# Optimization experiments

Hardware: AMD Instinct MI355X
Metric: run time of the kernel (lower is better)

Reference implementation:

```python
import jax, jax.numpy as jnp
import numpy as np

N, E, FIN, H, OUT, L = 80000, 1280000, 128, 64, 10, 3
NEG_SLOPE = 0.2


def setup_inputs() -> dict:
    key = jax.random.key(0)
    ks = jax.random.split(key, 2 + 6 * L + 2)
    inp = {
        "x": jax.random.normal(ks[0], (N, FIN), dtype=jnp.float32),
        "edge_index": jax.random.randint(ks[1], (2, E), 0, N, dtype=jnp.int32),
        "batch": jnp.zeros((N,), dtype=jnp.int32),
    }
    k = 2
    for l in range(L):
        fin = FIN if l == 0 else H
        s = 1.0 / np.sqrt(fin)
        inp[f"Wl{l}"] = jax.random.normal(ks[k + 0], (H, fin), dtype=jnp.float32) * s
        inp[f"bl{l}"] = jnp.zeros((H,), dtype=jnp.float32)
        inp[f"Wr{l}"] = jax.random.normal(ks[k + 1], (H, fin), dtype=jnp.float32) * s
        inp[f"br{l}"] = jnp.zeros((H,), dtype=jnp.float32)
        inp[f"att{l}"] = jax.random.normal(ks[k + 2], (H,), dtype=jnp.float32) * (1.0 / np.sqrt(H))
        inp[f"b{l}"] = jnp.zeros((H,), dtype=jnp.float32)
        k += 3
    inp["Wro"] = jax.random.normal(ks[k], (OUT, H), dtype=jnp.float32) * (1.0 / np.sqrt(H))
    inp["bro"] = jnp.zeros((OUT,), dtype=jnp.float32)
    return inp


def gatv2_layer(h, src, dst, Wl, bl, Wr, br, att, b):
    # PyG GATv2Conv (heads=1, share_weights=False):
    #   xl = lin_l(h) (source side), xr = lin_r(h) (target side)
    xl = h @ Wl.T + bl          # [N, H]
    xr = h @ Wr.T + br          # [N, H]
    e = jax.nn.leaky_relu(xl[src] + xr[dst], NEG_SLOPE) @ att  # [E_tot]
    # softmax over incoming edges of each destination node
    m = jax.ops.segment_max(e, dst, num_segments=N)
    ex = jnp.exp(e - m[dst])
    denom = jax.ops.segment_sum(ex, dst, num_segments=N)
    alpha = ex / denom[dst]
    out = jax.ops.segment_sum(alpha[:, None] * xl[src], dst, num_segments=N)
    return out + b


def reference(x, edge_index, batch,
              Wl0, bl0, Wr0, br0, att0, b0,
              Wl1, bl1, Wr1, br1, att1, b1,
              Wl2, bl2, Wr2, br2, att2, b2,
              Wro, bro):
    # add self-loops once (same augmented edge set used each layer)
    loop = jnp.arange(N, dtype=edge_index.dtype)
    src = jnp.concatenate([edge_index[0], loop])
    dst = jnp.concatenate([edge_index[1], loop])
    layers = [
        (Wl0, bl0, Wr0, br0, att0, b0),
        (Wl1, bl1, Wr1, br1, att1, b1),
        (Wl2, bl2, Wr2, br2, att2, b2),
    ]
    h = x
    for (Wl, bl, Wr, br, att, b) in layers:
        h = jax.nn.relu(gatv2_layer(h, src, dst, Wl, bl, Wr, br, att, b))
    # graph_level_task=False: node-level readout
    return h @ Wro.T + bro  # [N, OUT]
```

## Files before the change

kernel.cpp:

```cpp
#include <hip/hip_runtime.h>
#include <hip/hip_bf16.h>
#include <hip/hip_fp16.h>


#define NN 80000
#define EE 1280000
#define FIN 128
#define HH 64
#define OUTD 10
#define NBUK 79
#define PCH 2048
#define NCH 625

typedef __hip_bfloat16 bf16;
typedef _Float16 f16x8 __attribute__((ext_vector_type(8)));
typedef float f32x4 __attribute__((ext_vector_type(4)));

__device__ __forceinline__ float ldw(const void* p, int i, int f) {
    return f ? __bfloat162float(((const bf16*)p)[i]) : ((const float*)p)[i];
}

__global__ void detect_kernel(const unsigned* __restrict__ w, int* __restrict__ flag) {
    int lane = threadIdx.x;
    int big = 0;
    for (int i = lane; i < 2048; i += 64) {
        unsigned u = w[i];
        float a = __uint_as_float(u << 16);
        float b = __uint_as_float(u & 0xffff0000u);
        if (!(fabsf(a) <= 1024.f)) big = 1;
        if (!(fabsf(b) <= 1024.f)) big = 1;
    }
    big = (__ballot(big) != 0ull) ? 1 : 0;
    if (lane == 0) flag[0] = big ? 0 : 1;
}

__global__ void preconvert(
    const void* Wl0, const void* Wr0, const void* Wl1, const void* Wr1,
    const void* Wl2, const void* Wr2,
    const void* bl0, const void* br0, const void* bl1, const void* br1,
    const void* bl2, const void* br2,
    const void* att0, const void* att1, const void* att2,
    const void* b0, const void* b1, const void* b2,
    const void* Wro, const void* bro,
    __half* Wh0, __half* Wh1, __half* Wh2, float* small,
    const int* __restrict__ flagp)
{
    const int f = flagp[0];
    int t = blockIdx.x * 256 + threadIdx.x;
    if (t < 16384) {
        int j = t & 127, k = t >> 7;
        float v = (j < 64) ? ldw(Wl0, j * 128 + k, f) : ldw(Wr0, (j - 64) * 128 + k, f);
        Wh0[j * 128 + k] = __float2half(v);
    } else if (t < 24576) {
        int u = t - 16384; int j = u & 127, k = u >> 7;
        float v = (j < 64) ? ldw(Wl1, j * 64 + k, f) : ldw(Wr1, (j - 64) * 64 + k, f);
        Wh1[j * 64 + k] = __float2half(v);
    } else if (t < 32768) {
        int u = t - 24576; int j = u & 127, k = u >> 7;
        float v = (j < 64) ? ldw(Wl2, j * 64 + k, f) : ldw(Wr2, (j - 64) * 64 + k, f);
        Wh2[j * 64 + k] = __float2half(v);
    } else if (t < 34304) {
        int s = t - 32768;
        const void* BL[3] = { bl0, bl1, bl2 };
        const void* BR[3] = { br0, br1, br2 };
        const void* AT[3] = { att0, att1, att2 };
        const void* BB[3] = { b0, b1, b2 };
        float v = 0.f;
        if (s < 384) {
            int l = s / 128, r = s % 128;
            v = (r < 64) ? ldw(BL[l], r, f) : ldw(BR[l], r - 64, f);
        } else if (s < 576) {
            int q = s - 384; v = ldw(AT[q / 64], q % 64, f);
        } else if (s < 768) {
            int q = s - 576; v = ldw(BB[q / 64], q % 64, f);
        } else if (s < 1408) {
            v = ldw(Wro, s - 768, f);
        } else if (s < 1418) {
            v = ldw(bro, s - 1408, f);
        } else return;
        small[s] = v;
    }
}

__global__ __launch_bounds__(256) void chunkhist_kernel(const int* __restrict__ dst,
                                                        int* __restrict__ chunkcnt)
{
    __shared__ int h[NBUK];
    const int tid = threadIdx.x, c = blockIdx.x;
    for (int i = tid; i < NBUK; i += 256) h[i] = 0;
    __syncthreads();
    const int e0 = c * PCH + tid * 8;
    int4 a = *(const int4*)(dst + e0);
    int4 b = *(const int4*)(dst + e0 + 4);
    atomicAdd(&h[a.x >> 10], 1); atomicAdd(&h[a.y >> 10], 1);
    atomicAdd(&h[a.z >> 10], 1); atomicAdd(&h[a.w >> 10], 1);
    atomicAdd(&h[b.x >> 10], 1); atomicAdd(&h[b.y >> 10], 1);
    atomicAdd(&h[b.z >> 10], 1); atomicAdd(&h[b.w >> 10], 1);
    __syncthreads();
    for (int i = tid; i < NBUK; i += 256) chunkcnt[i * NCH + c] = h[i];
}

__global__ __launch_bounds__(1024) void cscan_kernel(int* __restrict__ chunkcnt,
                                                     int* __restrict__ bucket_cnt)
{
    __shared__ int s[1024];
    const int b = blockIdx.x, t = threadIdx.x;
    int v = (t < NCH) ? chunkcnt[b * NCH + t] : 0;
    s[t] = v;
    __syncthreads();
    #pragma unroll
    for (int off = 1; off < 1024; off <<= 1) {
        int u = (t >= off) ? s[t - off] : 0;
        __syncthreads();
        s[t] += u;
        __syncthreads();
    }
    if (t < NCH) chunkcnt[b * NCH + t] = s[t] - v;
    if (t == NCH - 1) bucket_cnt[b] = s[t];
}

__global__ void bscan_kernel(const int* __restrict__ bucket_cnt,
                             int* __restrict__ bucket_base)
{
    __shared__ int sc[128];
    const int t = threadIdx.x;
    sc[t] = (t < NBUK) ? bucket_cnt[t] : 0;
    __syncthreads();
    #pragma unroll
    for (int off = 1; off < 128; off <<= 1) {
        int v = (t >= off) ? sc[t - off] : 0;
        __syncthreads();
        sc[t] += v;
        __syncthreads();
    }
    if (t < NBUK) bucket_base[t] = (t == 0) ? 0 : sc[t - 1];
    if (t == 0) bucket_base[NBUK] = sc[NBUK - 1];
}

__global__ __launch_bounds__(256) void part_kernel(const int* __restrict__ src,
                                                   const int* __restrict__ dst,
                                                   const int* __restrict__ chunkcnt,
                                                   const int* __restrict__ bucket_base,
                                                   int2* __restrict__ part)
{
    __shared__ int hcnt[NBUK];
    __shared__ int sc[128];
    __shared__ int hbase[NBUK + 1];
    __shared__ int hpos[NBUK];
    __shared__ int hgb[NBUK];
    __shared__ int2 stage[PCH];
    const int tid = threadIdx.x, c = blockIdx.x;

    for (int i = tid; i < NBUK; i += 256) hcnt[i] = 0;
    __syncthreads();

    const int e0 = c * PCH + tid * 8;
    int4 sa = *(const int4*)(src + e0);
    int4 sb = *(const int4*)(src + e0 + 4);
    int4 da = *(const int4*)(dst + e0);
    int4 db = *(const int4*)(dst + e0 + 4);
    int dv[8] = { da.x, da.y, da.z, da.w, db.x, db.y, db.z, db.w };
    int sv[8] = { sa.x, sa.y, sa.z, sa.w, sb.x, sb.y, sb.z, sb.w };
    #pragma unroll
    for (int u = 0; u < 8; u++) atomicAdd(&hcnt[dv[u] >> 10], 1);
    __syncthreads();

    if (tid < 128) sc[tid] = (tid < NBUK) ? hcnt[tid] : 0;
    __syncthreads();
    #pragma unroll
    for (int off = 1; off < 128; off <<= 1) {
        int v = (tid < 128 && tid >= off) ? sc[tid - off] : 0;
        __syncthreads();
        if (tid < 128) sc[tid] += v;
        __syncthreads();
    }
    if (tid < NBUK) {
        int b = (tid == 0) ? 0 : sc[tid - 1];
        hbase[tid] = b;
        hpos[tid] = b;
        hgb[tid] = bucket_base[tid] + chunkcnt[tid * NCH + c];
    }
    if (tid == 0) hbase[NBUK] = PCH;
    __syncthreads();

    #pragma unroll
    for (int u = 0; u < 8; u++) {
        int p = atomicAdd(&hpos[dv[u] >> 10], 1);
        stage[p] = make_int2(sv[u], dv[u]);
    }
    __syncthreads();

    for (int s = tid; s < PCH; s += 256) {
        int lo = 0, hi = NBUK;
        #pragma unroll
        for (int it = 0; it < 7; it++) {
            int mid = (lo + hi) >> 1;
            if (hbase[mid] <= s) lo = mid; else hi = mid;
        }
        part[hgb[lo] + (s - hbase[lo])] = stage[s];
    }
}

__global__ __launch_bounds__(256) void hist_part_kernel(const int2* __restrict__ part,
                                                        const int* __restrict__ bucket_base,
                                                        int* __restrict__ cnt)
{
    __shared__ int lcnt[1024];
    const int b = blockIdx.x, tid = threadIdx.x;
    const int dbase = b << 10;
    for (int i = tid; i < 1024; i += 256) lcnt[i] = 0;
    __syncthreads();
    const int eb = bucket_base[b], ee = bucket_base[b + 1];
    for (int e = eb + tid; e < ee; e += 256)
        atomicAdd(&lcnt[part[e].y - dbase], 1);
    __syncthreads();
    const int nd = min(1024, NN - dbase);
    for (int i = tid; i < nd; i += 256) cnt[dbase + i] = lcnt[i];
}

__global__ void scan1(const int* __restrict__ cnt, int* __restrict__ rowptr,
                      int* __restrict__ bsums) {
    __shared__ int sh[256];
    int i = blockIdx.x * 256 + threadIdx.x;
    int tid = threadIdx.x;
    int c = (i < NN) ? cnt[i] : 0;
    sh[tid] = c;
    __syncthreads();
    #pragma unroll
    for (int off = 1; off < 256; off <<= 1) {
        int t = (tid >= off) ? sh[tid - off] : 0;
        __syncthreads();
        sh[tid] += t;
        __syncthreads();
    }
    if (i < NN) rowptr[i + 1] = sh[tid];
    if (tid == 255) bsums[blockIdx.x] = sh[255];
}

__global__ void scan2(int* __restrict__ bsums, int nb) {
    __shared__ int sh[512];
    int t = threadIdx.x;
    sh[t] = (t < nb) ? bsums[t] : 0;
    __syncthreads();
    #pragma unroll
    for (int off = 1; off < 512; off <<= 1) {
        int v = (t >= off) ? sh[t - off] : 0;
        __syncthreads();
        sh[t] += v;
        __syncthreads();
    }
    if (t < nb) bsums[t] = sh[t];
}

__global__ void scan3(int* __restrict__ rowptr, const int* __restrict__ bsums) {
    int i = blockIdx.x * 256 + threadIdx.x;
    if (i == 0) rowptr[0] = 0;
    int add = (blockIdx.x == 0) ? 0 : bsums[blockIdx.x - 1];
    if (i < NN) rowptr[i + 1] += add;
}

__global__ __launch_bounds__(256) void scatter2_kernel(const int2* __restrict__ part,
                                                       const int* __restrict__ bucket_base,
                                                       const int* __restrict__ rowptr,
                                                       int* __restrict__ col)
{
    __shared__ int lfill[1024];
    const int b = blockIdx.x, tid = threadIdx.x;
    const int dbase = b << 10;
    const int nd = min(1024, NN - dbase);
    for (int i = tid; i < nd; i += 256) lfill[i] = rowptr[dbase + i];
    __syncthreads();
    const int eb = bucket_base[b], ee = bucket_base[b + 1];
    for (int e = eb + tid; e < ee; e += 256) {
        int2 sd = part[e];
        int pos = atomicAdd(&lfill[sd.y - dbase], 1);
        col[pos] = sd.x;
    }
}

#define ELX_S 72
#define EXR_S 68
template<int F, bool L0>
__global__ __launch_bounds__(256) void lin_mfma(const void* __restrict__ hin_,
                                                const __half* __restrict__ Wh,
                                                const float* __restrict__ biasLR,
                                                const float* __restrict__ attf,
                                                __half* __restrict__ xlh,
                                                float* __restrict__ xr,
                                                float* __restrict__ slp,
                                                float* __restrict__ srp,
                                                const int* __restrict__ flagp)
{
    __shared__ __align__(16) char lds[64 * ELX_S * 2 + 64 * EXR_S * 4];
    _Float16* xs  = (_Float16*)lds;
    _Float16* eXL = (_Float16*)lds;
    float*    eXR = (float*)(lds + 64 * ELX_S * 2);

    const int tid = threadIdx.x;
    const int nb = blockIdx.x * 64;
    constexpr int OPR = F / 8;

    if (L0 && flagp[0]) {
        const uint4* hp = (const uint4*)hin_;
        for (int c = tid; c < 64 * OPR; c += 256) {
            int row = c / OPR, oct = c % OPR;
            uint4 u = hp[((size_t)(nb + row) * F + oct * 8) >> 3];
            unsigned ww[4] = { u.x, u.y, u.z, u.w };
            _Float16 v[8];
            #pragma unroll
            for (int p = 0; p < 4; p++) {
                v[2 * p]     = (_Float16)__uint_as_float(ww[p] << 16);
                v[2 * p + 1] = (_Float16)__uint_as_float(ww[p] & 0xffff0000u);
            }
            int so = oct ^ (row & 7);
            *(f16x8*)&xs[row * F + so * 8] = *(f16x8*)v;
        }
    } else {
        const float4* hp = (const float4*)hin_;
        for (int c = tid; c < 64 * OPR; c += 256) {
            int row = c / OPR, oct = c % OPR;
            size_t base = ((size_t)(nb + row) * F + oct * 8) >> 2;
            float4 a = hp[base], b = hp[base + 1];
            _Float16 v[8] = { (_Float16)a.x, (_Float16)a.y, (_Float16)a.z, (_Float16)a.w,
                              (_Float16)b.x, (_Float16)b.y, (_Float16)b.z, (_Float16)b.w };
            int so = oct ^ (row & 7);
            *(f16x8*)&xs[row * F + so * 8] = *(f16x8*)v;
        }
    }
    __syncthreads();

    const int w = tid >> 6;
    const int lane = tid & 63;
    const int n = lane & 15;
    const int quad = lane >> 4;
    constexpr int NS = F / 32;

    f16x8 afr[NS];
    #pragma unroll
    for (int s = 0; s < NS; s++) {
        int o = (s * 4 + quad) ^ (n & 7);
        afr[s] = *(const f16x8*)&xs[(w * 16 + n) * F + o * 8];
    }
    __syncthreads();

    const _Float16* Whf = (const _Float16*)Wh;
    #pragma unroll
    for (int ct = 0; ct < 8; ct++) {
        float bv = biasLR[ct * 16 + n];
        f32x4 acc = { bv, bv, bv, bv };
        #pragma unroll
        for (int s = 0; s < NS; s++) {
            f16x8 bfr = *(const f16x8*)&Whf[(size_t)(ct * 16 + n) * F + s * 32 + quad * 8];
            acc = __builtin_amdgcn_mfma_f32_16x16x32_f16(afr[s], bfr, acc, 0, 0, 0);
        }
        int rbase = w * 16 + quad * 4;
        if (ct < 4) {
            #pragma unroll
            for (int rg = 0; rg < 4; rg++)
                eXL[(rbase + rg) * ELX_S + ct * 16 + n] = (_Float16)acc[rg];
        } else {
            #pragma unroll
            for (int rg = 0; rg < 4; rg++)
                eXR[(rbase + rg) * EXR_S + (ct - 4) * 16 + n] = acc[rg];
        }
    }
    __syncthreads();

    for (int c = tid; c < 512; c += 256) {
        int row = c >> 3, oct = c & 7;
        *(uint4*)&xlh[(size_t)(nb + row) * 64 + oct * 8] =
            *(const uint4*)&eXL[row * ELX_S + oct * 8];
    }
    for (int c = tid; c < 1024; c += 256) {
        int row = c >> 4, q4 = c & 15;
        *(float4*)&xr[(size_t)(nb + row) * 64 + q4 * 4] =
            *(const float4*)&eXR[row * EXR_S + q4 * 4];
    }

    if (tid < 64) {
        float accl = 0.f, accr = 0.f;
        #pragma unroll
        for (int o = 0; o < 8; o++) {
            f16x8 vl = *(const f16x8*)&eXL[tid * ELX_S + o * 8];
            float4 a0 = *(const float4*)(attf + o * 8);
            float4 a1 = *(const float4*)(attf + o * 8 + 4);
            float4 v0 = *(const float4*)&eXR[tid * EXR_S + o * 8];
            float4 v1 = *(const float4*)&eXR[tid * EXR_S + o * 8 + 4];
            accl = fmaf(a0.x, (float)vl[0], accl);
            accl = fmaf(a0.y, (float)vl[1], accl);
            accl = fmaf(a0.z, (float)vl[2], accl);
            accl = fmaf(a0.w, (float)vl[3], accl);
            accl = fmaf(a1.x, (float)vl[4], accl);
            accl = fmaf(a1.y, (float)vl[5], accl);
            accl = fmaf(a1.z, (float)vl[6], accl);
            accl = fmaf(a1.w, (float)vl[7], accl);
            accr = fmaf(a0.x, v0.x, accr);
            accr = fmaf(a0.y, v0.y, accr);
            accr = fmaf(a0.z, v0.z, accr);
            accr = fmaf(a0.w, v0.w, accr);
            accr = fmaf(a1.x, v1.x, accr);
            accr = fmaf(a1.y, v1.y, accr);
            accr = fmaf(a1.z, v1.z, accr);
            accr = fmaf(a1.w, v1.w, accr);
        }
        slp[nb + tid] = accl;
        srp[nb + tid] = accr;
    }
}

#define DECODE8(U, D) { \
    float2 _f0 = __half22float2(*(__half2*)&U.x); \
    float2 _f1 = __half22float2(*(__half2*)&U.y); \
    float2 _f2 = __half22float2(*(__half2*)&U.z); \
    float2 _f3 = __half22float2(*(__half2*)&U.w); \
    D[0]=_f0.x; D[1]=_f0.y; D[2]=_f1.x; D[3]=_f1.y; \
    D[4]=_f2.x; D[5]=_f2.y; D[6]=_f3.x; D[7]=_f3.y; }

__global__ __launch_bounds__(256) void agg6_kernel(const __half* __restrict__ xlh,
                                                   const float* __restrict__ xr,
                                                   const float* __restrict__ slp,
                                                   const float* __restrict__ srp,
                                                   const float* __restrict__ attf,
                                                   const float* __restrict__ bf,
                                                   const int* __restrict__ rowptr,
                                                   const int* __restrict__ col,
                                                   float* __restrict__ hout)
{
    const int lane = threadIdx.x & 63;
    const int g = lane >> 3;
    const int r = lane & 7;
    const int wid = blockIdx.x * 4 + (threadIdx.x >> 6);
    const int i = wid * 8 + g;

    float xri[8], att[8];
    {
        float4 xa = *(const float4*)(xr + (size_t)i * 64 + r * 8);
        float4 xb = *(const float4*)(xr + (size_t)i * 64 + r * 8 + 4);
        xri[0]=xa.x; xri[1]=xa.y; xri[2]=xa.z; xri[3]=xa.w;
        xri[4]=xb.x; xri[5]=xb.y; xri[6]=xb.z; xri[7]=xb.w;
        float4 aa = *(const float4*)(attf + r * 8);
        float4 ab = *(const float4*)(attf + r * 8 + 4);
        att[0]=aa.x; att[1]=aa.y; att[2]=aa.z; att[3]=aa.w;
        att[4]=ab.x; att[5]=ab.y; att[6]=ab.z; att[7]=ab.w;
    }
    const float sri06 = 0.6f * srp[i];

    uint4 srow = *(const uint4*)(xlh + (size_t)i * 64 + r * 8);
    float s[8]; DECODE8(srow, s);
    float ps = 0.f;
    #pragma unroll
    for (int k = 0; k < 8; k++)
        ps = fmaf(att[k], fabsf(s[k] + xri[k]), ps);
    ps += __shfl_xor(ps, 1, 64);
    ps += __shfl_xor(ps, 2, 64);
    ps += __shfl_xor(ps, 4, 64);
    float es = fmaf(0.4f, ps, fmaf(0.6f, slp[i], sri06));
    float wself = __expf(fminf(es, 60.f));

    float acc[8];
    #pragma unroll
    for (int k = 0; k < 8; k++) acc[k] = wself * s[k];
    float denom = wself;

    const int e0 = rowptr[i], e1 = rowptr[i + 1];

    int e = e0;
    for (; e + 2 <= e1; e += 2) {
        int sa = col[e];
        int sb = col[e + 1];
        float sla = slp[sa], slb = slp[sb];
        uint4 ua = *(const uint4*)(xlh + (size_t)sa * 64 + r * 8);
        uint4 ub = *(const uint4*)(xlh + (size_t)sb * 64 + r * 8);
        float A[8], B[8];
        DECODE8(ua, A);
        DECODE8(ub, B);

        float pa = 0.f, pb = 0.f;
        #pragma unroll
        for (int k = 0; k < 8; k++) {
            pa = fmaf(att[k], fabsf(A[k] + xri[k]), pa);
            pb = fmaf(att[k], fabsf(B[k] + xri[k]), pb);
        }
        pa += __shfl_xor(pa, 1, 64);  pb += __shfl_xor(pb, 1, 64);
        pa += __shfl_xor(pa, 2, 64);  pb += __shfl_xor(pb, 2, 64);
        pa += __shfl_xor(pa, 4, 64);  pb += __shfl_xor(pb, 4, 64);

        float ea = fmaf(0.4f, pa, fmaf(0.6f, sla, sri06));
        float eb = fmaf(0.4f, pb, fmaf(0.6f, slb, sri06));
        float wa = __expf(fminf(ea, 60.f));
        float wb = __expf(fminf(eb, 60.f));

        #pragma unroll
        for (int k = 0; k < 8; k++) {
            acc[k] = fmaf(wa, A[k], acc[k]);
            acc[k] = fmaf(wb, B[k], acc[k]);
        }
        denom += wa + wb;
    }
    if (e < e1) {
        int sa = col[e];
        float sla = slp[sa];
        uint4 ua = *(const uint4*)(xlh + (size_t)sa * 64 + r * 8);
        float A[8];
        DECODE8(ua, A);

        float pa = 0.f;
        #pragma unroll
        for (int k = 0; k < 8; k++)
            pa = fmaf(att[k], fabsf(A[k] + xri[k]), pa);
        pa += __shfl_xor(pa, 1, 64);
        pa += __shfl_xor(pa, 2, 64);
        pa += __shfl_xor(pa, 4, 64);

        float ea = fmaf(0.4f, pa, fmaf(0.6f, sla, sri06));
        float wa = __expf(fminf(ea, 60.f));

        #pragma unroll
        for (int k = 0; k < 8; k++)
            acc[k] = fmaf(wa, A[k], acc[k]);
        denom += wa;
    }

    float inv = 1.f / denom;
    float4 bfa = *(const float4*)(bf + r * 8);
    float4 bfb = *(const float4*)(bf + r * 8 + 4);
    float o0 = fmaxf(fmaf(acc[0], inv, bfa.x), 0.f);
    float o1 = fmaxf(fmaf(acc[1], inv, bfa.y), 0.f);
    float o2 = fmaxf(fmaf(acc[2], inv, bfa.z), 0.f);
    float o3 = fmaxf(fmaf(acc[3], inv, bfa.w), 0.f);
    float o4 = fmaxf(fmaf(acc[4], inv, bfb.x), 0.f);
    float o5 = fmaxf(fmaf(acc[5], inv, bfb.y), 0.f);
    float o6 = fmaxf(fmaf(acc[6], inv, bfb.z), 0.f);
    float o7 = fmaxf(fmaf(acc[7], inv, bfb.w), 0.f);
    float* op = hout + (size_t)i * 64 + r * 8;
    *(float4*)(op)     = make_float4(o0, o1, o2, o3);
    *(float4*)(op + 4) = make_float4(o4, o5, o6, o7);
}

__global__ __launch_bounds__(256) void readout2_kernel(const float* __restrict__ h,
                                                       const float* __restrict__ WROf,
                                                       const float* __restrict__ brof,
                                                       void* __restrict__ out,
                                                       const int* __restrict__ flagp)
{
    __shared__ float wsh[640];
    __shared__ float bsh[OUTD];
    const int tid = threadIdx.x;
    for (int idx = tid; idx < 640; idx += 256) {
        int k = idx / 10, o = idx % 10;
        wsh[idx] = WROf[o * 64 + k];
    }
    if (tid < OUTD) bsh[tid] = brof[tid];
    __syncthreads();

    const int i = blockIdx.x * 256 + tid;
    if (i >= NN) return;
    const int f = flagp[0];

    float res[OUTD];
    #pragma unroll
    for (int o = 0; o < OUTD; o++) res[o] = bsh[o];

    const float4* h4 = (const float4*)(h + (size_t)i * 64);
    #pragma unroll 4
    for (int c = 0; c < 16; c++) {
        float4 hv = h4[c];
        const float* wp = &wsh[c * 40];
        #pragma unroll
        for (int o = 0; o < OUTD; o++) {
            float t = fmaf(hv.x, wp[o], fmaf(hv.y, wp[10 + o],
                      fmaf(hv.z, wp[20 + o], hv.w * wp[30 + o])));
            res[o] += t;
        }
    }

    if (f) {
        bf16* op = (bf16*)out + (size_t)i * OUTD;
        #pragma unroll
        for (int o = 0; o < OUTD; o++) op[o] = __float2bfloat16(res[o]);
    } else {
        float* op = (float*)out + (size_t)i * OUTD;
        #pragma unroll
        for (int o = 0; o < OUTD; o++) op[o] = res[o];
    }
}

extern "C" void kernel_launch(void* const* d_in, const int* in_sizes, int n_in,
                              void* d_out, int out_size, void* d_ws, size_t ws_size,
                              hipStream_t stream) {
    const void* x   = d_in[0];
    const int* ei   = (const int*)d_in[1];
    const void* Wl0 = d_in[3];  const void* bl0 = d_in[4];
    const void* Wr0 = d_in[5];  const void* br0 = d_in[6];
    const void* at0 = d_in[7];  const void* b0  = d_in[8];
    const void* Wl1 = d_in[9];  const void* bl1 = d_in[10];
    const void* Wr1 = d_in[11]; const void* br1 = d_in[12];
    const void* at1 = d_in[13]; const void* b1  = d_in[14];
    const void* Wl2 = d_in[15]; const void* bl2 = d_in[16];
    const void* Wr2 = d_in[17]; const void* br2 = d_in[18];
    const void* at2 = d_in[19]; const void* b2  = d_in[20];
    const void* Wro = d_in[21]; const void* bro = d_in[22];

    const int* srcArr = ei;
    const int* dstArr = ei + EE;

    float* wf = (float*)d_ws;
    __half* Wh0  = (__half*)wf;
    __half* Wh1  = (__half*)(wf + 16384);
    __half* Wh2  = (__half*)(wf + 24576);
    float* small = wf + 32768;
    int*   flag  = (int*)(wf + 34304);
    int*   rowptr = (int*)(wf + 34368);
    int*   bsums  = (int*)(wf + 114496);
    int*   fillc  = (int*)(wf + 115008);
    int*   bucket_cnt  = (int*)(wf + 195008);
    int*   bucket_base = (int*)(wf + 195136);
    int*   chunkcnt    = (int*)(wf + 195264);
    int2*  part   = (int2*)(wf + 244736);
    int*   col    = (int*)(wf + 2804736);
    float* slp    = wf + 4084736;
    float* srp    = wf + 4164736;
    __half* xlh   = (__half*)(wf + 5364736);
    float* xr = wf + 7924736;
    float* hA = xr + (size_t)NN * 64;

    float* biasLR0 = small;        float* biasLR1 = small + 128; float* biasLR2 = small + 256;
    float* attf0 = small + 384;    float* attf1 = small + 448;   float* attf2 = small + 512;
    float* bf0   = small + 576;    float* bf1   = small + 640;   float* bf2   = small + 704;
    float* WROf  = small + 768;    float* brof  = small + 1408;

    detect_kernel<<<dim3(1), dim3(64), 0, stream>>>((const unsigned*)Wl0, flag);

    preconvert<<<dim3(134), dim3(256), 0, stream>>>(
        Wl0, Wr0, Wl1, Wr1, Wl2, Wr2, bl0, br0, bl1, br1, bl2, br2,
        at0, at1, at2, b0, b1, b2, Wro, bro, Wh0, Wh1, Wh2, small, flag);

    chunkhist_kernel<<<dim3(NCH), dim3(256), 0, stream>>>(dstArr, chunkcnt);
    cscan_kernel<<<dim3(NBUK), dim3(1024), 0, stream>>>(chunkcnt, bucket_cnt);
    bscan_kernel<<<dim3(1), dim3(128), 0, stream>>>(bucket_cnt, bucket_base);
    part_kernel<<<dim3(NCH), dim3(256), 0, stream>>>(srcArr, dstArr, chunkcnt, bucket_base, part);
    hist_part_kernel<<<dim3(NBUK), dim3(256), 0, stream>>>(part, bucket_base, fillc);
    scan1<<<dim3(313), dim3(256), 0, stream>>>(fillc, rowptr, bsums);
    scan2<<<dim3(1), dim3(512), 0, stream>>>(bsums, 313);
    scan3<<<dim3(313), dim3(256), 0, stream>>>(rowptr, bsums);
    scatter2_kernel<<<dim3(NBUK), dim3(256), 0, stream>>>(part, bucket_base, rowptr, col);

    lin_mfma<128, true><<<dim3(NN / 64), dim3(256), 0, stream>>>(x, Wh0, biasLR0, attf0, xlh, xr, slp, srp, flag);
    agg6_kernel<<<dim3(NN / 32), dim3(256), 0, stream>>>(xlh, xr, slp, srp, attf0, bf0, rowptr, col, hA);
    lin_mfma<64, false><<<dim3(NN / 64), dim3(256), 0, stream>>>(hA, Wh1, biasLR1, attf1, xlh, xr, slp, srp, flag);
    agg6_kernel<<<dim3(NN / 32), dim3(256), 0, stream>>>(xlh, xr, slp, srp, attf1, bf1, rowptr, col, hA);
    lin_mfma<64, false><<<dim3(NN / 64), dim3(256), 0, stream>>>(hA, Wh2, biasLR2, attf2, xlh, xr, slp, srp, flag);
    agg6_kernel<<<dim3(NN / 32), dim3(256), 0, stream>>>(xlh, xr, slp, srp, attf2, bf2, rowptr, col, hA);

    readout2_kernel<<<dim3(313), dim3(256), 0, stream>>>(hA, WROf, brof, d_out, flag);
}
```

Measured before the change: 379.4 us.

## Replace bucketed CSR build with global atomics and degree-sorted node order

Drops the multi-kernel chunk/bucket partition pipeline and builds the CSR with a global-atomic histogram followed by an atomic scatter of edges into rows. It also bins nodes by in-degree (descending) during the scan and produces an order array, so each aggregation wavefront processes nodes of similar degree and load imbalance within a wave is reduced. The cost is heavily contended global atomics, column order within each row that is no longer deterministic, and scattered writes and reads of node outputs through the permutation.

```diff
diff --git a/kernel.cpp b/kernel.cpp
--- a/kernel.cpp
+++ b/kernel.cpp
@@ -8,9 +8,6 @@
 #define FIN 128
 #define HH 64
 #define OUTD 10
-#define NBUK 79
-#define PCH 2048
-#define NCH 625
 
 typedef __hip_bfloat16 bf16;
 typedef _Float16 f16x8 __attribute__((ext_vector_type(8)));
@@ -82,150 +79,34 @@
     }
 }
 
-__global__ __launch_bounds__(256) void chunkhist_kernel(const int* __restrict__ dst,
-                                                        int* __restrict__ chunkcnt)
-{
-    __shared__ int h[NBUK];
-    const int tid = threadIdx.x, c = blockIdx.x;
-    for (int i = tid; i < NBUK; i += 256) h[i] = 0;
-    __syncthreads();
-    const int e0 = c * PCH + tid * 8;
-    int4 a = *(const int4*)(dst + e0);
-    int4 b = *(const int4*)(dst + e0 + 4);
-    atomicAdd(&h[a.x >> 10], 1); atomicAdd(&h[a.y >> 10], 1);
-    atomicAdd(&h[a.z >> 10], 1); atomicAdd(&h[a.w >> 10], 1);
-    atomicAdd(&h[b.x >> 10], 1); atomicAdd(&h[b.y >> 10], 1);
-    atomicAdd(&h[b.z >> 10], 1); atomicAdd(&h[b.w >> 10], 1);
-    __syncthreads();
-    for (int i = tid; i < NBUK; i += 256) chunkcnt[i * NCH + c] = h[i];
-}
-
-__global__ __launch_bounds__(1024) void cscan_kernel(int* __restrict__ chunkcnt,
-                                                     int* __restrict__ bucket_cnt)
-{
-    __shared__ int s[1024];
-    const int b = blockIdx.x, t = threadIdx.x;
-    int v = (t < NCH) ? chunkcnt[b * NCH + t] : 0;
-    s[t] = v;
-    __syncthreads();
-    #pragma unroll
-    for (int off = 1; off < 1024; off <<= 1) {
-        int u = (t >= off) ? s[t - off] : 0;
-        __syncthreads();
-        s[t] += u;
-        __syncthreads();
-    }
-    if (t < NCH) chunkcnt[b * NCH + t] = s[t] - v;
-    if (t == NCH - 1) bucket_cnt[b] = s[t];
-}
-
-__global__ void bscan_kernel(const int* __restrict__ bucket_cnt,
-                             int* __restrict__ bucket_base)
-{
-    __shared__ int sc[128];
-    const int t = threadIdx.x;
-    sc[t] = (t < NBUK) ? bucket_cnt[t] : 0;
-    __syncthreads();
-    #pragma unroll
-    for (int off = 1; off < 128; off <<= 1) {
-        int v = (t >= off) ? sc[t - off] : 0;
-        __syncthreads();
-        sc[t] += v;
-        __syncthreads();
-    }
-    if (t < NBUK) bucket_base[t] = (t == 0) ? 0 : sc[t - 1];
-    if (t == 0) bucket_base[NBUK] = sc[NBUK - 1];
-}
-
-__global__ __launch_bounds__(256) void part_kernel(const int* __restrict__ src,
-                                                   const int* __restrict__ dst,
-                                                   const int* __restrict__ chunkcnt,
-                                                   const int* __restrict__ bucket_base,
-                                                   int2* __restrict__ part)
-{
-    __shared__ int hcnt[NBUK];
-    __shared__ int sc[128];
-    __shared__ int hbase[NBUK + 1];
-    __shared__ int hpos[NBUK];
-    __shared__ int hgb[NBUK];
-    __shared__ int2 stage[PCH];
-    const int tid = threadIdx.x, c = blockIdx.x;
-
-    for (int i = tid; i < NBUK; i += 256) hcnt[i] = 0;
-    __syncthreads();
-
-    const int e0 = c * PCH + tid * 8;
-    int4 sa = *(const int4*)(src + e0);
-    int4 sb = *(const int4*)(src + e0 + 4);
-    int4 da = *(const int4*)(dst + e0);
-    int4 db = *(const int4*)(dst + e0 + 4);
-    int dv[8] = { da.x, da.y, da.z, da.w, db.x, db.y, db.z, db.w };
-    int sv[8] = { sa.x, sa.y, sa.z, sa.w, sb.x, sb.y, sb.z, sb.w };
-    #pragma unroll
-    for (int u = 0; u < 8; u++) atomicAdd(&hcnt[dv[u] >> 10], 1);
-    __syncthreads();
-
-    if (tid < 128) sc[tid] = (tid < NBUK) ? hcnt[tid] : 0;
-    __syncthreads();
-    #pragma unroll
-    for (int off = 1; off < 128; off <<= 1) {
-        int v = (tid < 128 && tid >= off) ? sc[tid - off] : 0;
-        __syncthreads();
-        if (tid < 128) sc[tid] += v;
-        __syncthreads();
-    }
-    if (tid < NBUK) {
-        int b = (tid == 0) ? 0 : sc[tid - 1];
-        hbase[tid] = b;
-        hpos[tid] = b;
-        hgb[tid] = bucket_base[tid] + chunkcnt[tid * NCH + c];
-    }
-    if (tid == 0) hbase[NBUK] = PCH;
-    __syncthreads();
-
-    #pragma unroll
-    for (int u = 0; u < 8; u++) {
-        int p = atomicAdd(&hpos[dv[u] >> 10], 1);
-        stage[p] = make_int2(sv[u], dv[u]);
-    }
-    __syncthreads();
-
-    for (int s = tid; s < PCH; s += 256) {
-        int lo = 0, hi = NBUK;
-        #pragma unroll
-        for (int it = 0; it < 7; it++) {
-            int mid = (lo + hi) >> 1;
-            if (hbase[mid] <= s) lo = mid; else hi = mid;
-        }
-        part[hgb[lo] + (s - hbase[lo])] = stage[s];
-    }
-}
-
-__global__ __launch_bounds__(256) void hist_part_kernel(const int2* __restrict__ part,
-                                                        const int* __restrict__ bucket_base,
-                                                        int* __restrict__ cnt)
-{
-    __shared__ int lcnt[1024];
-    const int b = blockIdx.x, tid = threadIdx.x;
-    const int dbase = b << 10;
-    for (int i = tid; i < 1024; i += 256) lcnt[i] = 0;
-    __syncthreads();
-    const int eb = bucket_base[b], ee = bucket_base[b + 1];
-    for (int e = eb + tid; e < ee; e += 256)
-        atomicAdd(&lcnt[part[e].y - dbase], 1);
-    __syncthreads();
-    const int nd = min(1024, NN - dbase);
-    for (int i = tid; i < nd; i += 256) cnt[dbase + i] = lcnt[i];
+__global__ void zero_kernel(int* __restrict__ fillc, int* __restrict__ dbin) {
+    int i = blockIdx.x * 256 + threadIdx.x;
+    if (i < NN) fillc[i] = 0;
+    if (i < 64) dbin[i] = 0;
+}
+
+__global__ __launch_bounds__(256) void hist_kernel(const int* __restrict__ dst,
+                                                   int* __restrict__ fillc)
+{
+    int e = (blockIdx.x * 256 + threadIdx.x) * 4;
+    int4 d = *(const int4*)(dst + e);
+    atomicAdd(&fillc[d.x], 1);
+    atomicAdd(&fillc[d.y], 1);
+    atomicAdd(&fillc[d.z], 1);
+    atomicAdd(&fillc[d.w], 1);
 }
 
 __global__ void scan1(const int* __restrict__ cnt, int* __restrict__ rowptr,
-                      int* __restrict__ bsums) {
+                      int* __restrict__ bsums, int* __restrict__ dbin) {
     __shared__ int sh[256];
+    __shared__ int lb[64];
     int i = blockIdx.x * 256 + threadIdx.x;
     int tid = threadIdx.x;
+    if (tid < 64) lb[tid] = 0;
     int c = (i < NN) ? cnt[i] : 0;
     sh[tid] = c;
     __syncthreads();
+    if (i < NN) atomicAdd(&lb[63 - min(c, 63)], 1);
     #pragma unroll
     for (int off = 1; off < 256; off <<= 1) {
         int t = (tid >= off) ? sh[tid - off] : 0;
@@ -235,12 +116,16 @@
     }
     if (i < NN) rowptr[i + 1] = sh[tid];
     if (tid == 255) bsums[blockIdx.x] = sh[255];
-}
-
-__global__ void scan2(int* __restrict__ bsums, int nb) {
+    __syncthreads();
+    if (tid < 64 && lb[tid]) atomicAdd(&dbin[tid], lb[tid]);
+}
+
+__global__ void scan2(int* __restrict__ bsums, int nb, int* __restrict__ dbin) {
     __shared__ int sh[512];
+    __shared__ int db[64];
     int t = threadIdx.x;
     sh[t] = (t < nb) ? bsums[t] : 0;
+    if (t < 64) db[t] = dbin[t];
     __syncthreads();
     #pragma unroll
     for (int off = 1; off < 512; off <<= 1) {
@@ -250,6 +135,15 @@
         __syncthreads();
     }
     if (t < nb) bsums[t] = sh[t];
+    int own = (t < 64) ? db[t] : 0;
+    #pragma unroll
+    for (int off = 1; off < 64; off <<= 1) {
+        int v = (t < 64 && t >= off) ? db[t - off] : 0;
+        __syncthreads();
+        if (t < 64) db[t] += v;
+        __syncthreads();
+    }
+    if (t < 64) dbin[t] = db[t] - own;
 }
 
 __global__ void scan3(int* __restrict__ rowptr, const int* __restrict__ bsums) {
@@ -259,23 +153,33 @@
     if (i < NN) rowptr[i + 1] += add;
 }
 
-__global__ __launch_bounds__(256) void scatter2_kernel(const int2* __restrict__ part,
-                                                       const int* __restrict__ bucket_base,
-                                                       const int* __restrict__ rowptr,
+__global__ void prep_kernel(const int* __restrict__ fillc,
+                            const int* __restrict__ rowptr,
+                            int* __restrict__ dbin,
+                            int* __restrict__ wfill,
+                            int* __restrict__ order)
+{
+    int i = blockIdx.x * 256 + threadIdx.x;
+    if (i >= NN) return;
+    wfill[i] = rowptr[i];
+    int b = 63 - min(fillc[i], 63);
+    int p = atomicAdd(&dbin[b], 1);
+    order[p] = i;
+}
+
+__global__ __launch_bounds__(256) void escatter_kernel(const int* __restrict__ src,
+                                                       const int* __restrict__ dst,
+                                                       int* __restrict__ wfill,
                                                        int* __restrict__ col)
 {
-    __shared__ int lfill[1024];
-    const int b = blockIdx.x, tid = threadIdx.x;
-    const int dbase = b << 10;
-    const int nd = min(1024, NN - dbase);
-    for (int i = tid; i < nd; i += 256) lfill[i] = rowptr[dbase + i];
-    __syncthreads();
-    const int eb = bucket_base[b], ee = bucket_base[b + 1];
-    for (int e = eb + tid; e < ee; e += 256) {
-        int2 sd = part[e];
-        int pos = atomicAdd(&lfill[sd.y - dbase], 1);
-        col[pos] = sd.x;
-    }
+    int e = (blockIdx.x * 256 + threadIdx.x) * 4;
+    int4 s = *(const int4*)(src + e);
+    int4 d = *(const int4*)(dst + e);
+    int p;
+    p = atomicAdd(&wfill[d.x], 1); col[p] = s.x;
+    p = atomicAdd(&wfill[d.y], 1); col[p] = s.y;
+    p = atomicAdd(&wfill[d.z], 1); col[p] = s.z;
+    p = atomicAdd(&wfill[d.w], 1); col[p] = s.w;
 }
 
 #define ELX_S 72
@@ -416,7 +320,7 @@
     D[0]=_f0.x; D[1]=_f0.y; D[2]=_f1.x; D[3]=_f1.y; \
     D[4]=_f2.x; D[5]=_f2.y; D[6]=_f3.x; D[7]=_f3.y; }
 
-__global__ __launch_bounds__(256) void agg6_kernel(const __half* __restrict__ xlh,
+__global__ __launch_bounds__(256) void agg7_kernel(const __half* __restrict__ xlh,
                                                    const float* __restrict__ xr,
                                                    const float* __restrict__ slp,
                                                    const float* __restrict__ srp,
@@ -424,13 +328,14 @@
                                                    const float* __restrict__ bf,
                                                    const int* __restrict__ rowptr,
                                                    const int* __restrict__ col,
+                                                   const int* __restrict__ order,
                                                    float* __restrict__ hout)
 {
     const int lane = threadIdx.x & 63;
     const int g = lane >> 3;
     const int r = lane & 7;
     const int wid = blockIdx.x * 4 + (threadIdx.x >> 6);
-    const int i = wid * 8 + g;
+    const int i = order[wid * 8 + g];
 
     float xri[8], att[8];
     {
@@ -613,11 +518,10 @@
     int*   rowptr = (int*)(wf + 34368);
     int*   bsums  = (int*)(wf + 114496);
     int*   fillc  = (int*)(wf + 115008);
-    int*   bucket_cnt  = (int*)(wf + 195008);
-    int*   bucket_base = (int*)(wf + 195136);
-    int*   chunkcnt    = (int*)(wf + 195264);
-    int2*  part   = (int2*)(wf + 244736);
-    int*   col    = (int*)(wf + 2804736);
+    int*   wfill  = (int*)(wf + 195008);
+    int*   dbin   = (int*)(wf + 275008);
+    int*   order  = (int*)(wf + 275136);
+    int*   col    = (int*)(wf + 355200);
     float* slp    = wf + 4084736;
     float* srp    = wf + 4164736;
     __half* xlh   = (__half*)(wf + 5364736);
@@ -635,22 +539,20 @@
         Wl0, Wr0, Wl1, Wr1, Wl2, Wr2, bl0, br0, bl1, br1, bl2, br2,
         at0, at1, at2, b0, b1, b2, Wro, bro, Wh0, Wh1, Wh2, small, flag);
 
-    chunkhist_kernel<<<dim3(NCH), dim3(256), 0, stream>>>(dstArr, chunkcnt);
-    cscan_kernel<<<dim3(NBUK), dim3(1024), 0, stream>>>(chunkcnt, bucket_cnt);
-    bscan_kernel<<<dim3(1), dim3(128), 0, stream>>>(bucket_cnt, bucket_base);
-    part_kernel<<<dim3(NCH), dim3(256), 0, stream>>>(srcArr, dstArr, chunkcnt, bucket_base, part);
-    hist_part_kernel<<<dim3(NBUK), dim3(256), 0, stream>>>(part, bucket_base, fillc);
-    scan1<<<dim3(313), dim3(256), 0, stream>>>(fillc, rowptr, bsums);
-    scan2<<<dim3(1), dim3(512), 0, stream>>>(bsums, 313);
+    zero_kernel<<<dim3(313), dim3(256), 0, stream>>>(fillc, dbin);
+    hist_kernel<<<dim3(EE / 1024), dim3(256), 0, stream>>>(dstArr, fillc);
+    scan1<<<dim3(313), dim3(256), 0, stream>>>(fillc, rowptr, bsums, dbin);
+    scan2<<<dim3(1), dim3(512), 0, stream>>>(bsums, 313, dbin);
     scan3<<<dim3(313), dim3(256), 0, stream>>>(rowptr, bsums);
-    scatter2_kernel<<<dim3(NBUK), dim3(256), 0, stream>>>(part, bucket_base, rowptr, col);
+    prep_kernel<<<dim3(313), dim3(256), 0, stream>>>(fillc, rowptr, dbin, wfill, order);
+    escatter_kernel<<<dim3(EE / 1024), dim3(256), 0, stream>>>(srcArr, dstArr, wfill, col);
 
     lin_mfma<128, true><<<dim3(NN / 64), dim3(256), 0, stream>>>(x, Wh0, biasLR0, attf0, xlh, xr, slp, srp, flag);
-    agg6_kernel<<<dim3(NN / 32), dim3(256), 0, stream>>>(xlh, xr, slp, srp, attf0, bf0, rowptr, col, hA);
+    agg7_kernel<<<dim3(NN / 32), dim3(256), 0, stream>>>(xlh, xr, slp, srp, attf0, bf0, rowptr, col, order, hA);
     lin_mfma<64, false><<<dim3(NN / 64), dim3(256), 0, stream>>>(hA, Wh1, biasLR1, attf1, xlh, xr, slp, srp, flag);
-    agg6_kernel<<<dim3(NN / 32), dim3(256), 0, stream>>>(xlh, xr, slp, srp, attf1, bf1, rowptr, col, hA);
+    agg7_kernel<<<dim3(NN / 32), dim3(256), 0, stream>>>(xlh, xr, slp, srp, attf1, bf1, rowptr, col, order, hA);
     lin_mfma<64, false><<<dim3(NN / 64), dim3(256), 0, stream>>>(hA, Wh2, biasLR2, attf2, xlh, xr, slp, srp, flag);
-    agg6_kernel<<<dim3(NN / 32), dim3(256), 0, stream>>>(xlh, xr, slp, srp, attf2, bf2, rowptr, col, hA);
+    agg7_kernel<<<dim3(NN / 32), dim3(256), 0, stream>>>(xlh, xr, slp, srp, attf2, bf2, rowptr, col, order, hA);
 
     readout2_kernel<<<dim3(313), dim3(256), 0, stream>>>(hA, WROf, brof, d_out, flag);
 }
```

Result: slower. 674.9 us (+77.9%).

## Sort destination nodes by degree within windows to balance aggregation warps

Applied to the files above, without the earlier changes.

Adds a kernel that, within windows of 2000 nodes, counting-sorts node indices by in-degree (descending, capped at 63). The aggregation kernel then processes nodes in that order, so the 8 nodes sharing a wavefront have similar edge counts. This is meant to reduce divergence and idle lanes from degree imbalance. In exchange it adds one small kernel, an extra indirection load, and less sequential access to xr, srp and hout.

```diff
diff --git a/kernel.cpp b/kernel.cpp
--- a/kernel.cpp
+++ b/kernel.cpp
@@ -11,6 +11,7 @@
 #define NBUK 79
 #define PCH 2048
 #define NCH 625
+#define WND 2000
 
 typedef __hip_bfloat16 bf16;
 typedef _Float16 f16x8 __attribute__((ext_vector_type(8)));
@@ -259,6 +260,41 @@
     if (i < NN) rowptr[i + 1] += add;
 }
 
+__global__ __launch_bounds__(256) void wprep_kernel(const int* __restrict__ fillc,
+                                                    int* __restrict__ order)
+{
+    __shared__ int h[64];
+    const int w0 = blockIdx.x * WND;
+    const int tid = threadIdx.x;
+    if (tid < 64) h[tid] = 0;
+    __syncthreads();
+    int bin[8];
+    #pragma unroll
+    for (int u = 0; u < 8; u++) {
+        int t = tid + u * 256;
+        if (t < WND) {
+            int b = 63 - min(fillc[w0 + t], 63);
+            bin[u] = b;
+            atomicAdd(&h[b], 1);
+        } else bin[u] = -1;
+    }
+    __syncthreads();
+    if (tid == 0) {
+        int run = 0;
+        #pragma unroll
+        for (int b = 0; b < 64; b++) { int c = h[b]; h[b] = run; run += c; }
+    }
+    __syncthreads();
+    #pragma unroll
+    for (int u = 0; u < 8; u++) {
+        int t = tid + u * 256;
+        if (t < WND) {
+            int p = atomicAdd(&h[bin[u]], 1);
+            order[w0 + p] = w0 + t;
+        }
+    }
+}
+
 __global__ __launch_bounds__(256) void scatter2_kernel(const int2* __restrict__ part,
                                                        const int* __restrict__ bucket_base,
                                                        const int* __restrict__ rowptr,
@@ -416,7 +452,7 @@
     D[0]=_f0.x; D[1]=_f0.y; D[2]=_f1.x; D[3]=_f1.y; \
     D[4]=_f2.x; D[5]=_f2.y; D[6]=_f3.x; D[7]=_f3.y; }
 
-__global__ __launch_bounds__(256) void agg6_kernel(const __half* __restrict__ xlh,
+__global__ __launch_bounds__(256) void agg7_kernel(const __half* __restrict__ xlh,
                                                    const float* __restrict__ xr,
                                                    const float* __restrict__ slp,
                                                    const float* __restrict__ srp,
@@ -424,13 +460,14 @@
                                                    const float* __restrict__ bf,
                                                    const int* __restrict__ rowptr,
                                                    const int* __restrict__ col,
+                                                   const int* __restrict__ order,
                                                    float* __restrict__ hout)
 {
     const int lane = threadIdx.x & 63;
     const int g = lane >> 3;
     const int r = lane & 7;
     const int wid = blockIdx.x * 4 + (threadIdx.x >> 6);
-    const int i = wid * 8 + g;
+    const int i = order[wid * 8 + g];
 
     float xri[8], att[8];
     {
@@ -620,6 +657,7 @@
     int*   col    = (int*)(wf + 2804736);
     float* slp    = wf + 4084736;
     float* srp    = wf + 4164736;
+    int*   order  = (int*)(wf + 4244736);
     __half* xlh   = (__half*)(wf + 5364736);
     float* xr = wf + 7924736;
     float* hA = xr + (size_t)NN * 64;
@@ -643,14 +681,15 @@
     scan1<<<dim3(313), dim3(256), 0, stream>>>(fillc, rowptr, bsums);
     scan2<<<dim3(1), dim3(512), 0, stream>>>(bsums, 313);
     scan3<<<dim3(313), dim3(256), 0, stream>>>(rowptr, bsums);
+    wprep_kernel<<<dim3(NN / WND), dim3(256), 0, stream>>>(fillc, order);
     scatter2_kernel<<<dim3(NBUK), dim3(256), 0, stream>>>(part, bucket_base, rowptr, col);
 
     lin_mfma<128, true><<<dim3(NN / 64), dim3(256), 0, stream>>>(x, Wh0, biasLR0, attf0, xlh, xr, slp, srp, flag);
-    agg6_kernel<<<dim3(NN / 32), dim3(256), 0, stream>>>(xlh, xr, slp, srp, attf0, bf0, rowptr, col, hA);
+    agg7_kernel<<<dim3(NN / 32), dim3(256), 0, stream>>>(xlh, xr, slp, srp, attf0, bf0, rowptr, col, order, hA);
     lin_mfma<64, false><<<dim3(NN / 64), dim3(256), 0, stream>>>(hA, Wh1, biasLR1, attf1, xlh, xr, slp, srp, flag);
-    agg6_kernel<<<dim3(NN / 32), dim3(256), 0, stream>>>(xlh, xr, slp, srp, attf1, bf1, rowptr, col, hA);
+    agg7_kernel<<<dim3(NN / 32), dim3(256), 0, stream>>>(xlh, xr, slp, srp, attf1, bf1, rowptr, col, order, hA);
     lin_mfma<64, false><<<dim3(NN / 64), dim3(256), 0, stream>>>(hA, Wh2, biasLR2, attf2, xlh, xr, slp, srp, flag);
-    agg6_kernel<<<dim3(NN / 32), dim3(256), 0, stream>>>(xlh, xr, slp, srp, attf2, bf2, rowptr, col, hA);
+    agg7_kernel<<<dim3(NN / 32), dim3(256), 0, stream>>>(xlh, xr, slp, srp, attf2, bf2, rowptr, col, order, hA);
 
     readout2_kernel<<<dim3(313), dim3(256), 0, stream>>>(hA, WROf, brof, d_out, flag);
 }
```

Measured after the change: 393.8 us. +3.8%, slower.
